# Kernel optimization log

Hardware: AMD Instinct MI355X
Metric: run time of the kernel (lower is better)

The kernel has to match this reference:

```python
import jax, jax.numpy as jnp
import numpy as np

N_SRC, N_DST, E, T, C = 10000, 10000, 320000, 4, 64


def setup_inputs() -> dict:
    key = jax.random.key(0)
    ks = jax.random.split(key, 8)
    return {
        "feat_src": jax.random.normal(ks[0], (N_SRC, T, C), dtype=jnp.float32),
        "feat_dst": jax.random.normal(ks[1], (N_DST, T, C), dtype=jnp.float32),
        "edge_weight": jax.random.uniform(ks[2], (E,), dtype=jnp.float32),
        "weight_e": jax.random.normal(ks[3], (1, C), dtype=jnp.float32) * (6.0 / (1 + C)) ** 0.5,
        "u": jax.random.normal(ks[4], (C, C), dtype=jnp.float32) * (3.0 / C) ** 0.5,
        "v": jax.random.normal(ks[5], (C, C), dtype=jnp.float32) * (3.0 / C) ** 0.5,
        "ln_gamma": jnp.ones((C,), dtype=jnp.float32),
        "ln_beta": jnp.zeros((C,), dtype=jnp.float32),
        "src_idx": jax.random.randint(ks[6], (E,), 0, N_SRC, dtype=jnp.int32),
        "dst_idx": jax.random.randint(ks[7], (E,), 0, N_DST, dtype=jnp.int32),
    }


def reference(feat_src, feat_dst, edge_weight, weight_e, u, v, ln_gamma, ln_beta, src_idx, dst_idx):
    n_dst = feat_dst.shape[0]
    # edge feature projection: [E] -> [E,1] @ [1,C] -> [E,C]
    ew = edge_weight[:, None] @ weight_e
    # node projections: [N,T,C] @ [C,C]
    h_src = jnp.einsum('ntc,cd->ntd', feat_src, u)
    h_dst = jnp.einsum('ntc,cd->ntd', feat_dst, v)
    # per-edge gather
    hs = h_src[src_idx]              # [E,T,C]
    hd = h_dst[dst_idx]              # [E,T,C]
    gate = jax.nn.sigmoid(hs * hd * ew[:, None, :])  # [E,T,C]
    msg = hs * gate                  # [E,T,C]
    # scatter-sum over destination nodes
    aggr = jax.ops.segment_sum(msg, dst_idx, num_segments=n_dst)  # [N_dst,T,C]
    out = jnp.einsum('ntc,cd->ntd', feat_dst, u) + aggr
    # LayerNorm over last dim (normalize == 'ln')
    mean = out.mean(axis=-1, keepdims=True)
    var = out.var(axis=-1, keepdims=True)
    out = (out - mean) * jax.lax.rsqrt(var + 1e-5) * ln_gamma + ln_beta
    return out + feat_dst
```

## Files before the change

kernel.cpp:

```cpp
#include <hip/hip_runtime.h>
#include <math.h>


#define BUCKET 80

__device__ __forceinline__ unsigned short f2bf(float f) {
    unsigned u = __float_as_uint(f);
    return (unsigned short)((u + 0x7fffu + ((u >> 16) & 1u)) >> 16);
}

__global__ __launch_bounds__(256) void init_kernel(
    int* __restrict__ counts, int n_dst, int2* __restrict__ es, int es_total,
    ushort4* __restrict__ h_srcT, int n_src) {
    int i = blockIdx.x * 256 + threadIdx.x;
    if (i < n_dst) counts[i] = 0;
    if (i < 64) h_srcT[(size_t)n_src * 64 + i] = make_ushort4(0, 0, 0, 0);
    if (i < es_total) es[i] = make_int2(n_src << 6, 0);
}

__global__ __launch_bounds__(256) void proj_kernel(
    const float* __restrict__ feat_src, const float* __restrict__ feat_dst,
    const float* __restrict__ U, const float* __restrict__ V,
    const float* __restrict__ weight_e,
    const int* __restrict__ src_idx, const int* __restrict__ dst_idx,
    const float* __restrict__ ew, int E,
    ushort4* __restrict__ h_srcT, float* __restrict__ h_base, float* __restrict__ h_dst_w,
    int* __restrict__ counts, int2* __restrict__ es,
    int n_src, int n_dst, int nsb) {
    __shared__ float sA[128 * 68];
    __shared__ float sW[4096];
    int t = threadIdx.x, b = blockIdx.x;

    for (int e = b * 256 + t; e < E; e += gridDim.x * 256) {
        int d = dst_idx[e];
        int pos = atomicAdd(&counts[d], 1);
        if (pos < BUCKET)
            es[d * BUCKET + pos] = make_int2(src_idx[e] << 6, __float_as_int(ew[e]));
    }

    int type = (b < nsb) ? 0 : (b < 2 * nsb) ? 1 : 2;
    int rb = b - type * nsb;
    int nrows = (type == 0 ? n_src : n_dst) * 4;
    int r0 = rb * 128;
    const float* A = (type == 0) ? feat_src : feat_dst;
    const float* W = (type == 2) ? V : U;

    {
        const float4* W4 = (const float4*)W;
        float4* sW4 = (float4*)sW;
#pragma unroll
        for (int i = 0; i < 4; ++i) sW4[t + i * 256] = W4[t + i * 256];
    }
    {
        int row = t >> 4, chunk = t & 15;
#pragma unroll
        for (int p = 0; p < 8; ++p) {
            int rr = row + p * 16;
            int r = r0 + rr;
            if (r >= nrows) r = nrows - 1;
            float4 v = *(const float4*)(A + (size_t)r * 64 + chunk * 4);
            *(float4*)&sA[rr * 68 + chunk * 4] = v;
        }
    }
    __syncthreads();

    int rg = t >> 4;
    int c4 = (t & 15) * 4;
    int rowbase = rg * 8;

    float acc[8][4] = {};
#pragma unroll 2
    for (int k4 = 0; k4 < 64; k4 += 4) {
        float4 av[8];
#pragma unroll
        for (int j = 0; j < 8; ++j)
            av[j] = *(const float4*)&sA[(rowbase + j) * 68 + k4];
#pragma unroll
        for (int q = 0; q < 4; ++q) {
            float4 wu = *(const float4*)&sW[(k4 + q) * 64 + c4];
#pragma unroll
            for (int j = 0; j < 8; ++j) {
                float a = q == 0 ? av[j].x : q == 1 ? av[j].y : q == 2 ? av[j].z : av[j].w;
                acc[j][0] = fmaf(a, wu.x, acc[j][0]);
                acc[j][1] = fmaf(a, wu.y, acc[j][1]);
                acc[j][2] = fmaf(a, wu.z, acc[j][2]);
                acc[j][3] = fmaf(a, wu.w, acc[j][3]);
            }
        }
    }

    if (type == 0) {
#pragma unroll
        for (int half = 0; half < 2; ++half) {
            int node = (r0 >> 2) + rg * 2 + half;
            if (node < n_src) {
#pragma unroll
                for (int m = 0; m < 4; ++m) {
                    ushort4 st;
                    st.x = f2bf(acc[half * 4 + 0][m]);
                    st.y = f2bf(acc[half * 4 + 1][m]);
                    st.z = f2bf(acc[half * 4 + 2][m]);
                    st.w = f2bf(acc[half * 4 + 3][m]);
                    h_srcT[(size_t)node * 64 + c4 + m] = st;
                }
            }
        }
    } else if (type == 1) {
#pragma unroll
        for (int j = 0; j < 8; ++j) {
            int r = r0 + rowbase + j;
            if (r < nrows) {
                float4 su;
                su.x = acc[j][0]; su.y = acc[j][1]; su.z = acc[j][2]; su.w = acc[j][3];
                *(float4*)&h_base[(size_t)r * 64 + c4] = su;
            }
        }
    } else {
        const float nl2e = -1.44269504f;
        float4 we = *(const float4*)&weight_e[c4];
        float wm0 = we.x * nl2e, wm1 = we.y * nl2e, wm2 = we.z * nl2e, wm3 = we.w * nl2e;
#pragma unroll
        for (int j = 0; j < 8; ++j) {
            int r = r0 + rowbase + j;
            if (r < nrows) {
                float4 sv;
                sv.x = acc[j][0] * wm0; sv.y = acc[j][1] * wm1;
                sv.z = acc[j][2] * wm2; sv.w = acc[j][3] * wm3;
                *(float4*)&h_dst_w[(size_t)r * 64 + c4] = sv;
            }
        }
    }
}

__global__ __launch_bounds__(256) void aggregate_kernel(
    const ushort4* __restrict__ h_srcT,
    const float* __restrict__ h_dst_w, const float* __restrict__ h_base,
    const float* __restrict__ feat_dst,
    const int* __restrict__ counts, const int2* __restrict__ es,
    const float* __restrict__ gamma, const float* __restrict__ beta,
    float* __restrict__ out) {
    __shared__ float xbuf[4][4][64];
    int tid = threadIdx.x;
    int w = tid >> 6, c = tid & 63;
    int d = blockIdx.x;
    size_t rb = (size_t)d * 256;

    float hw0 = h_dst_w[rb +   0 + c];
    float hw1 = h_dst_w[rb +  64 + c];
    float hw2 = h_dst_w[rb + 128 + c];
    float hw3 = h_dst_w[rb + 192 + c];

    int ngroups = (counts[d] + 3) >> 2;
    const int2* ep = es + d * BUCKET;

    float acc0 = 0.f, acc1 = 0.f, acc2 = 0.f, acc3 = 0.f;

    ushort4 hA[4]; float wA[4];
    int g = w;
#pragma unroll
    for (int i = 0; i < 4; ++i) {
        int2 ev = ep[4 * g + i];
        wA[i] = __int_as_float(ev.y);
        hA[i] = h_srcT[ev.x + c];
    }
    while (g < ngroups) {
        int gn = g + 4;
        ushort4 hB[4]; float wB[4];
#pragma unroll
        for (int i = 0; i < 4; ++i) {
            int2 ev = ep[4 * gn + i];
            wB[i] = __int_as_float(ev.y);
            hB[i] = h_srcT[ev.x + c];
        }
#pragma unroll
        for (int i = 0; i < 4; ++i) {
            float ww = wA[i];
            float x0 = __uint_as_float((unsigned)hA[i].x << 16);
            float x1 = __uint_as_float((unsigned)hA[i].y << 16);
            float x2 = __uint_as_float((unsigned)hA[i].z << 16);
            float x3 = __uint_as_float((unsigned)hA[i].w << 16);
            float g0 = __builtin_amdgcn_rcpf(1.f + __builtin_amdgcn_exp2f(x0 * (hw0 * ww)));
            float g1 = __builtin_amdgcn_rcpf(1.f + __builtin_amdgcn_exp2f(x1 * (hw1 * ww)));
            float g2 = __builtin_amdgcn_rcpf(1.f + __builtin_amdgcn_exp2f(x2 * (hw2 * ww)));
            float g3 = __builtin_amdgcn_rcpf(1.f + __builtin_amdgcn_exp2f(x3 * (hw3 * ww)));
            acc0 = fmaf(x0, g0, acc0);
            acc1 = fmaf(x1, g1, acc1);
            acc2 = fmaf(x2, g2, acc2);
            acc3 = fmaf(x3, g3, acc3);
        }
#pragma unroll
        for (int i = 0; i < 4; ++i) { hA[i] = hB[i]; wA[i] = wB[i]; }
        g = gn;
    }

    xbuf[w][0][c] = acc0;
    xbuf[w][1][c] = acc1;
    xbuf[w][2][c] = acc2;
    xbuf[w][3][c] = acc3;
    __syncthreads();
    float f = xbuf[0][w][c] + xbuf[1][w][c] + xbuf[2][w][c] + xbuf[3][w][c]
            + h_base[rb + w * 64 + c];

    float s1 = f, s2 = f * f;
#pragma unroll
    for (int off = 32; off >= 1; off >>= 1) {
        s1 += __shfl_xor(s1, off, 64);
        s2 += __shfl_xor(s2, off, 64);
    }
    const float inv64 = 1.f / 64.f;
    float mean = s1 * inv64;
    float var  = s2 * inv64 - mean * mean;
    float inv  = rsqrtf(var + 1e-5f);
    out[rb + w * 64 + c] = (f - mean) * inv * gamma[c] + beta[c] + feat_dst[rb + w * 64 + c];
}

extern "C" void kernel_launch(void* const* d_in, const int* in_sizes, int n_in,
                              void* d_out, int out_size, void* d_ws, size_t ws_size,
                              hipStream_t stream) {
    const float* feat_src    = (const float*)d_in[0];
    const float* feat_dst    = (const float*)d_in[1];
    const float* edge_weight = (const float*)d_in[2];
    const float* weight_e    = (const float*)d_in[3];
    const float* u           = (const float*)d_in[4];
    const float* v           = (const float*)d_in[5];
    const float* ln_gamma    = (const float*)d_in[6];
    const float* ln_beta     = (const float*)d_in[7];
    const int*   src_idx     = (const int*)d_in[8];
    const int*   dst_idx     = (const int*)d_in[9];
    float* out = (float*)d_out;

    int E     = in_sizes[2];
    int n_src = in_sizes[0] / 256;
    int n_dst = in_sizes[1] / 256;

    int es_total = n_dst * BUCKET + 32;

    ushort4* h_srcT  = (ushort4*)d_ws;
    float* h_base    = (float*)(h_srcT + (size_t)(n_src + 1) * 64);
    float* h_dst_w   = h_base + (size_t)n_dst * 256;
    int2*  es        = (int2*)(h_dst_w + (size_t)n_dst * 256);
    int*   counts    = (int*)(es + es_total);

    int nsb = (n_src * 4 + 127) / 128;

    init_kernel<<<(es_total + 255) / 256, 256, 0, stream>>>(counts, n_dst, es, es_total,
                                                            h_srcT, n_src);
    proj_kernel<<<3 * nsb, 256, 0, stream>>>(feat_src, feat_dst, u, v, weight_e,
                                             src_idx, dst_idx, edge_weight, E,
                                             h_srcT, h_base, h_dst_w,
                                             counts, es, n_src, n_dst, nsb);
    aggregate_kernel<<<n_dst, 256, 0, stream>>>(h_srcT, h_dst_w, h_base,
                                                feat_dst, counts, es,
                                                ln_gamma, ln_beta, out);
}
```

Measured before the change: 78.33 us.

## Split edge bucketing into its own kernel and shrink projection tiles

Edge bucketing (atomic placement into per-destination buckets) moves out of the projection kernel into a separate place_kernel launch. The projection kernel now uses 64-row tiles with 4 rows per thread, a register double-buffer prefetch of the A operand from shared memory, and launch_bounds(256,4). This aims to raise occupancy and block count and to stop atomic scatter work from stalling the GEMM blocks. The cost is an extra kernel launch, and the edge scatter can no longer overlap with the projection.

```diff
diff --git a/kernel.cpp b/kernel.cpp
--- a/kernel.cpp
+++ b/kernel.cpp
@@ -18,30 +18,33 @@
     if (i < es_total) es[i] = make_int2(n_src << 6, 0);
 }
 
-__global__ __launch_bounds__(256) void proj_kernel(
-    const float* __restrict__ feat_src, const float* __restrict__ feat_dst,
-    const float* __restrict__ U, const float* __restrict__ V,
-    const float* __restrict__ weight_e,
+__global__ __launch_bounds__(256) void place_kernel(
     const int* __restrict__ src_idx, const int* __restrict__ dst_idx,
     const float* __restrict__ ew, int E,
-    ushort4* __restrict__ h_srcT, float* __restrict__ h_base, float* __restrict__ h_dst_w,
-    int* __restrict__ counts, int2* __restrict__ es,
-    int n_src, int n_dst, int nsb) {
-    __shared__ float sA[128 * 68];
-    __shared__ float sW[4096];
-    int t = threadIdx.x, b = blockIdx.x;
-
-    for (int e = b * 256 + t; e < E; e += gridDim.x * 256) {
+    int* __restrict__ counts, int2* __restrict__ es) {
+    int e = blockIdx.x * 256 + threadIdx.x;
+    if (e < E) {
         int d = dst_idx[e];
         int pos = atomicAdd(&counts[d], 1);
         if (pos < BUCKET)
             es[d * BUCKET + pos] = make_int2(src_idx[e] << 6, __float_as_int(ew[e]));
     }
+}
+
+__global__ __launch_bounds__(256, 4) void proj_kernel(
+    const float* __restrict__ feat_src, const float* __restrict__ feat_dst,
+    const float* __restrict__ U, const float* __restrict__ V,
+    const float* __restrict__ weight_e,
+    ushort4* __restrict__ h_srcT, float* __restrict__ h_base, float* __restrict__ h_dst_w,
+    int n_src, int n_dst, int nsb) {
+    __shared__ float sA[64 * 68];
+    __shared__ float sW[4096];
+    int t = threadIdx.x, b = blockIdx.x;
 
     int type = (b < nsb) ? 0 : (b < 2 * nsb) ? 1 : 2;
     int rb = b - type * nsb;
     int nrows = (type == 0 ? n_src : n_dst) * 4;
-    int r0 = rb * 128;
+    int r0 = rb * 64;
     const float* A = (type == 0) ? feat_src : feat_dst;
     const float* W = (type == 2) ? V : U;
 
@@ -54,7 +57,7 @@
     {
         int row = t >> 4, chunk = t & 15;
 #pragma unroll
-        for (int p = 0; p < 8; ++p) {
+        for (int p = 0; p < 4; ++p) {
             int rr = row + p * 16;
             int r = r0 + rr;
             if (r >= nrows) r = nrows - 1;
@@ -66,49 +69,50 @@
 
     int rg = t >> 4;
     int c4 = (t & 15) * 4;
-    int rowbase = rg * 8;
-
-    float acc[8][4] = {};
-#pragma unroll 2
+
+    float acc[4][4] = {};
+    float4 avA[4], avB[4];
+#pragma unroll
+    for (int j = 0; j < 4; ++j) avA[j] = *(const float4*)&sA[(rg * 4 + j) * 68 + 0];
+
+#pragma unroll
     for (int k4 = 0; k4 < 64; k4 += 4) {
-        float4 av[8];
-#pragma unroll
-        for (int j = 0; j < 8; ++j)
-            av[j] = *(const float4*)&sA[(rowbase + j) * 68 + k4];
+        if (k4 < 60) {
+#pragma unroll
+            for (int j = 0; j < 4; ++j)
+                avB[j] = *(const float4*)&sA[(rg * 4 + j) * 68 + k4 + 4];
+        }
 #pragma unroll
         for (int q = 0; q < 4; ++q) {
             float4 wu = *(const float4*)&sW[(k4 + q) * 64 + c4];
 #pragma unroll
-            for (int j = 0; j < 8; ++j) {
-                float a = q == 0 ? av[j].x : q == 1 ? av[j].y : q == 2 ? av[j].z : av[j].w;
+            for (int j = 0; j < 4; ++j) {
+                float a = q == 0 ? avA[j].x : q == 1 ? avA[j].y : q == 2 ? avA[j].z : avA[j].w;
                 acc[j][0] = fmaf(a, wu.x, acc[j][0]);
                 acc[j][1] = fmaf(a, wu.y, acc[j][1]);
                 acc[j][2] = fmaf(a, wu.z, acc[j][2]);
                 acc[j][3] = fmaf(a, wu.w, acc[j][3]);
             }
         }
+#pragma unroll
+        for (int j = 0; j < 4; ++j) avA[j] = avB[j];
     }
 
     if (type == 0) {
-#pragma unroll
-        for (int half = 0; half < 2; ++half) {
-            int node = (r0 >> 2) + rg * 2 + half;
-            if (node < n_src) {
-#pragma unroll
-                for (int m = 0; m < 4; ++m) {
-                    ushort4 st;
-                    st.x = f2bf(acc[half * 4 + 0][m]);
-                    st.y = f2bf(acc[half * 4 + 1][m]);
-                    st.z = f2bf(acc[half * 4 + 2][m]);
-                    st.w = f2bf(acc[half * 4 + 3][m]);
-                    h_srcT[(size_t)node * 64 + c4 + m] = st;
-                }
+        int node = (r0 >> 2) + rg;
+        if (node < n_src) {
+#pragma unroll
+            for (int m = 0; m < 4; ++m) {
+                ushort4 st;
+                st.x = f2bf(acc[0][m]); st.y = f2bf(acc[1][m]);
+                st.z = f2bf(acc[2][m]); st.w = f2bf(acc[3][m]);
+                h_srcT[(size_t)node * 64 + c4 + m] = st;
             }
         }
     } else if (type == 1) {
 #pragma unroll
-        for (int j = 0; j < 8; ++j) {
-            int r = r0 + rowbase + j;
+        for (int j = 0; j < 4; ++j) {
+            int r = r0 + rg * 4 + j;
             if (r < nrows) {
                 float4 su;
                 su.x = acc[j][0]; su.y = acc[j][1]; su.z = acc[j][2]; su.w = acc[j][3];
@@ -120,8 +124,8 @@
         float4 we = *(const float4*)&weight_e[c4];
         float wm0 = we.x * nl2e, wm1 = we.y * nl2e, wm2 = we.z * nl2e, wm3 = we.w * nl2e;
 #pragma unroll
-        for (int j = 0; j < 8; ++j) {
-            int r = r0 + rowbase + j;
+        for (int j = 0; j < 4; ++j) {
+            int r = r0 + rg * 4 + j;
             if (r < nrows) {
                 float4 sv;
                 sv.x = acc[j][0] * wm0; sv.y = acc[j][1] * wm1;
@@ -241,14 +245,15 @@
     int2*  es        = (int2*)(h_dst_w + (size_t)n_dst * 256);
     int*   counts    = (int*)(es + es_total);
 
-    int nsb = (n_src * 4 + 127) / 128;
+    int nsb = (n_src * 4 + 63) / 64;
 
     init_kernel<<<(es_total + 255) / 256, 256, 0, stream>>>(counts, n_dst, es, es_total,
                                                             h_srcT, n_src);
+    place_kernel<<<(E + 255) / 256, 256, 0, stream>>>(src_idx, dst_idx, edge_weight, E,
+                                                      counts, es);
     proj_kernel<<<3 * nsb, 256, 0, stream>>>(feat_src, feat_dst, u, v, weight_e,
-                                             src_idx, dst_idx, edge_weight, E,
                                              h_srcT, h_base, h_dst_w,
-                                             counts, es, n_src, n_dst, nsb);
+                                             n_src, n_dst, nsb);
     aggregate_kernel<<<n_dst, 256, 0, stream>>>(h_srcT, h_dst_w, h_base,
                                                 feat_dst, counts, es,
                                                 ln_gamma, ln_beta, out);
```

New measurement: 83.75 us. 1.07x slower.

## Use bf16 MFMA for node projections with prepacked weight fragments

Applied to the files above, without the earlier changes.

Replaces the shared-memory FP32 FMA tiling GEMM in the projection kernel with bf16 MFMA 16x16x32 instructions. U and V are converted to bf16 and laid out as MFMA B-fragments once, in the init kernel, so each wave loads them straight from global memory. The A rows are converted to bf16 in registers, which removes the shared memory and the block barrier. This lowers precision of the projections to bf16 inputs, and the new store pattern writes scalar floats instead of float4, so stores are less coalesced.

```diff
diff --git a/kernel.cpp b/kernel.cpp
--- a/kernel.cpp
+++ b/kernel.cpp
@@ -3,6 +3,9 @@
 
 
 #define BUCKET 80
+
+typedef short short8 __attribute__((ext_vector_type(8)));
+typedef float f32x4  __attribute__((ext_vector_type(4)));
 
 __device__ __forceinline__ unsigned short f2bf(float f) {
     unsigned u = __float_as_uint(f);
@@ -11,24 +14,35 @@
 
 __global__ __launch_bounds__(256) void init_kernel(
     int* __restrict__ counts, int n_dst, int2* __restrict__ es, int es_total,
-    ushort4* __restrict__ h_srcT, int n_src) {
+    ushort4* __restrict__ h_srcT, int n_src,
+    const float* __restrict__ U, const float* __restrict__ V,
+    short8* __restrict__ wfrag) {
     int i = blockIdx.x * 256 + threadIdx.x;
     if (i < n_dst) counts[i] = 0;
     if (i < 64) h_srcT[(size_t)n_src * 64 + i] = make_ushort4(0, 0, 0, 0);
     if (i < es_total) es[i] = make_int2(n_src << 6, 0);
+    if (i < 1024) {
+        int l = i & 63, ct = (i >> 6) & 3, kc = (i >> 8) & 1, mat = (i >> 9) & 1;
+        const float* W = mat ? V : U;
+        int col = ct * 16 + (l & 15);
+        int k0  = kc * 32 + (l >> 4) * 8;
+        short8 s;
+#pragma unroll
+        for (int j = 0; j < 8; ++j)
+            s[j] = (short)f2bf(W[(size_t)(k0 + j) * 64 + col]);
+        wfrag[i] = s;
+    }
 }
 
 __global__ __launch_bounds__(256) void proj_kernel(
     const float* __restrict__ feat_src, const float* __restrict__ feat_dst,
-    const float* __restrict__ U, const float* __restrict__ V,
     const float* __restrict__ weight_e,
     const int* __restrict__ src_idx, const int* __restrict__ dst_idx,
     const float* __restrict__ ew, int E,
+    const short8* __restrict__ wfrag,
     ushort4* __restrict__ h_srcT, float* __restrict__ h_base, float* __restrict__ h_dst_w,
     int* __restrict__ counts, int2* __restrict__ es,
     int n_src, int n_dst, int nsb) {
-    __shared__ float sA[128 * 68];
-    __shared__ float sW[4096];
     int t = threadIdx.x, b = blockIdx.x;
 
     for (int e = b * 256 + t; e < E; e += gridDim.x * 256) {
@@ -41,92 +55,76 @@
     int type = (b < nsb) ? 0 : (b < 2 * nsb) ? 1 : 2;
     int rb = b - type * nsb;
     int nrows = (type == 0 ? n_src : n_dst) * 4;
-    int r0 = rb * 128;
     const float* A = (type == 0) ? feat_src : feat_dst;
-    const float* W = (type == 2) ? V : U;
-
-    {
-        const float4* W4 = (const float4*)W;
-        float4* sW4 = (float4*)sW;
-#pragma unroll
-        for (int i = 0; i < 4; ++i) sW4[t + i * 256] = W4[t + i * 256];
-    }
-    {
-        int row = t >> 4, chunk = t & 15;
-#pragma unroll
-        for (int p = 0; p < 8; ++p) {
-            int rr = row + p * 16;
-            int r = r0 + rr;
-            if (r >= nrows) r = nrows - 1;
-            float4 v = *(const float4*)(A + (size_t)r * 64 + chunk * 4);
-            *(float4*)&sA[rr * 68 + chunk * 4] = v;
-        }
-    }
-    __syncthreads();
-
-    int rg = t >> 4;
-    int c4 = (t & 15) * 4;
-    int rowbase = rg * 8;
-
-    float acc[8][4] = {};
-#pragma unroll 2
-    for (int k4 = 0; k4 < 64; k4 += 4) {
-        float4 av[8];
-#pragma unroll
-        for (int j = 0; j < 8; ++j)
-            av[j] = *(const float4*)&sA[(rowbase + j) * 68 + k4];
-#pragma unroll
-        for (int q = 0; q < 4; ++q) {
-            float4 wu = *(const float4*)&sW[(k4 + q) * 64 + c4];
-#pragma unroll
-            for (int j = 0; j < 8; ++j) {
-                float a = q == 0 ? av[j].x : q == 1 ? av[j].y : q == 2 ? av[j].z : av[j].w;
-                acc[j][0] = fmaf(a, wu.x, acc[j][0]);
-                acc[j][1] = fmaf(a, wu.y, acc[j][1]);
-                acc[j][2] = fmaf(a, wu.z, acc[j][2]);
-                acc[j][3] = fmaf(a, wu.w, acc[j][3]);
-            }
-        }
-    }
-
-    if (type == 0) {
-#pragma unroll
-        for (int half = 0; half < 2; ++half) {
-            int node = (r0 >> 2) + rg * 2 + half;
+
+    int w = t >> 6, l = t & 63;
+    int lr = l & 15, lg = l >> 4;
+
+    const short8* wf = wfrag + (type == 2 ? 512 : 0);
+    short8 bf[2][4];
+#pragma unroll
+    for (int kc = 0; kc < 2; ++kc)
+#pragma unroll
+        for (int ct = 0; ct < 4; ++ct)
+            bf[kc][ct] = wf[(kc * 4 + ct) * 64 + l];
+
+#pragma unroll
+    for (int e2 = 0; e2 < 2; ++e2) {
+        int rs = rb * 128 + w * 32 + e2 * 16;
+        int rr = rs + lr; if (rr >= nrows) rr = nrows - 1;
+
+        short8 af[2];
+#pragma unroll
+        for (int kc = 0; kc < 2; ++kc) {
+            const float* ap = A + (size_t)rr * 64 + kc * 32 + lg * 8;
+            float4 a0 = *(const float4*)ap;
+            float4 a1 = *(const float4*)(ap + 4);
+            short8 s;
+            s[0] = (short)f2bf(a0.x); s[1] = (short)f2bf(a0.y);
+            s[2] = (short)f2bf(a0.z); s[3] = (short)f2bf(a0.w);
+            s[4] = (short)f2bf(a1.x); s[5] = (short)f2bf(a1.y);
+            s[6] = (short)f2bf(a1.z); s[7] = (short)f2bf(a1.w);
+            af[kc] = s;
+        }
+
+        f32x4 acc[4];
+#pragma unroll
+        for (int ct = 0; ct < 4; ++ct) { acc[ct][0]=0.f; acc[ct][1]=0.f; acc[ct][2]=0.f; acc[ct][3]=0.f; }
+#pragma unroll
+        for (int ct = 0; ct < 4; ++ct) {
+            acc[ct] = __builtin_amdgcn_mfma_f32_16x16x32_bf16(af[0], bf[0][ct], acc[ct], 0, 0, 0);
+            acc[ct] = __builtin_amdgcn_mfma_f32_16x16x32_bf16(af[1], bf[1][ct], acc[ct], 0, 0, 0);
+        }
+
+        if (type == 0) {
+            int node = (rs >> 2) + lg;
             if (node < n_src) {
 #pragma unroll
-                for (int m = 0; m < 4; ++m) {
+                for (int ct = 0; ct < 4; ++ct) {
                     ushort4 st;
-                    st.x = f2bf(acc[half * 4 + 0][m]);
-                    st.y = f2bf(acc[half * 4 + 1][m]);
-                    st.z = f2bf(acc[half * 4 + 2][m]);
-                    st.w = f2bf(acc[half * 4 + 3][m]);
-                    h_srcT[(size_t)node * 64 + c4 + m] = st;
+                    st.x = f2bf(acc[ct][0]); st.y = f2bf(acc[ct][1]);
+                    st.z = f2bf(acc[ct][2]); st.w = f2bf(acc[ct][3]);
+                    h_srcT[(size_t)node * 64 + ct * 16 + lr] = st;
                 }
             }
-        }
-    } else if (type == 1) {
-#pragma unroll
-        for (int j = 0; j < 8; ++j) {
-            int r = r0 + rowbase + j;
-            if (r < nrows) {
-                float4 su;
-                su.x = acc[j][0]; su.y = acc[j][1]; su.z = acc[j][2]; su.w = acc[j][3];
-                *(float4*)&h_base[(size_t)r * 64 + c4] = su;
-            }
-        }
-    } else {
-        const float nl2e = -1.44269504f;
-        float4 we = *(const float4*)&weight_e[c4];
-        float wm0 = we.x * nl2e, wm1 = we.y * nl2e, wm2 = we.z * nl2e, wm3 = we.w * nl2e;
-#pragma unroll
-        for (int j = 0; j < 8; ++j) {
-            int r = r0 + rowbase + j;
-            if (r < nrows) {
-                float4 sv;
-                sv.x = acc[j][0] * wm0; sv.y = acc[j][1] * wm1;
-                sv.z = acc[j][2] * wm2; sv.w = acc[j][3] * wm3;
-                *(float4*)&h_dst_w[(size_t)r * 64 + c4] = sv;
+        } else if (type == 1) {
+#pragma unroll
+            for (int ct = 0; ct < 4; ++ct)
+#pragma unroll
+                for (int q = 0; q < 4; ++q) {
+                    int r = rs + lg * 4 + q;
+                    if (r < nrows) h_base[(size_t)r * 64 + ct * 16 + lr] = acc[ct][q];
+                }
+        } else {
+            const float nl2e = -1.44269504f;
+#pragma unroll
+            for (int ct = 0; ct < 4; ++ct) {
+                float wm = weight_e[ct * 16 + lr] * nl2e;
+#pragma unroll
+                for (int q = 0; q < 4; ++q) {
+                    int r = rs + lg * 4 + q;
+                    if (r < nrows) h_dst_w[(size_t)r * 64 + ct * 16 + lr] = acc[ct][q] * wm;
+                }
             }
         }
     }
@@ -239,15 +237,16 @@
     float* h_base    = (float*)(h_srcT + (size_t)(n_src + 1) * 64);
     float* h_dst_w   = h_base + (size_t)n_dst * 256;
     int2*  es        = (int2*)(h_dst_w + (size_t)n_dst * 256);
-    int*   counts    = (int*)(es + es_total);
+    short8* wfrag    = (short8*)(es + es_total);
+    int*   counts    = (int*)(wfrag + 1024);
 
     int nsb = (n_src * 4 + 127) / 128;
 
     init_kernel<<<(es_total + 255) / 256, 256, 0, stream>>>(counts, n_dst, es, es_total,
-                                                            h_srcT, n_src);
-    proj_kernel<<<3 * nsb, 256, 0, stream>>>(feat_src, feat_dst, u, v, weight_e,
+                                                            h_srcT, n_src, u, v, wfrag);
+    proj_kernel<<<3 * nsb, 256, 0, stream>>>(feat_src, feat_dst, weight_e,
                                              src_idx, dst_idx, edge_weight, E,
-                                             h_srcT, h_base, h_dst_w,
+                                             wfrag, h_srcT, h_base, h_dst_w,
                                              counts, es, n_src, n_dst, nsb);
     aggregate_kernel<<<n_dst, 256, 0, stream>>>(h_srcT, h_dst_w, h_base,
                                                 feat_dst, counts, es,
```

Measured after the change: 70.35 us. 1.11x faster.
